# Kernel optimization log

Hardware: AMD Instinct MI355X
Metric: run time of the kernel (lower is better)

The kernel has to match this reference:

```python
import jax, jax.numpy as jnp
import numpy as np


def setup_inputs() -> dict:
    key = jax.random.key(0)
    ks = jax.random.split(key, 7)
    B, T, F, H = 512, 512, 64, 128
    s = 1.0 / np.sqrt(H)
    return {
        "x": jax.random.normal(ks[0], (B, T, F), dtype=jnp.float32),
        "W_ih": jax.random.uniform(ks[1], (3 * H, F), jnp.float32, -s, s),
        "W_hh": jax.random.uniform(ks[2], (3 * H, H), jnp.float32, -s, s),
        "b_ih": jax.random.uniform(ks[3], (3 * H,), jnp.float32, -s, s),
        "b_hh": jax.random.uniform(ks[4], (3 * H,), jnp.float32, -s, s),
        "W_out": jax.random.uniform(ks[5], (1, H), jnp.float32, -s, s),
        "b_out": jax.random.uniform(ks[6], (1,), jnp.float32, -s, s),
    }


def reference(x, W_ih, W_hh, b_ih, b_hh, W_out, b_out):
    B, T, F = x.shape
    H = W_hh.shape[1]
    # Precompute input projections for all timesteps: [T, B, 3H]
    x_t = jnp.transpose(x, (1, 0, 2))
    gi_all = jnp.einsum('tbf,gf->tbg', x_t, W_ih) + b_ih
    h0 = jnp.zeros((B, H), dtype=x.dtype)

    def step(h, gi):
        gh = h @ W_hh.T + b_hh  # [B, 3H]
        i_r, i_z, i_n = jnp.split(gi, 3, axis=-1)
        h_r, h_z, h_n = jnp.split(gh, 3, axis=-1)
        r = jax.nn.sigmoid(i_r + h_r)
        z = jax.nn.sigmoid(i_z + h_z)
        n = jnp.tanh(i_n + r * h_n)
        h_new = (1.0 - z) * n + z * h
        out = jnp.tanh(h_new @ W_out.T + b_out)[:, 0]  # [B]
        return h_new, out

    _, outs = jax.lax.scan(step, h0, gi_all)  # outs: [T, B]
    return outs.T  # [B, T]
```

## Files before the change

kernel.cpp:

```cpp
#include <hip/hip_runtime.h>
#include <math.h>

#define TSEQ 512
#define FDIM 64
#define HDIM 128
#define NB   512

#define SR 1.4426950408889634f
#define SN 2.8853900817779268f

typedef _Float16 f16x8 __attribute__((ext_vector_type(8)));
typedef _Float16 f16x4 __attribute__((ext_vector_type(4)));
typedef __fp16  fp16x2 __attribute__((ext_vector_type(2)));
typedef __attribute__((ext_vector_type(4))) float f32x4;

#define H_ROW 136
#define H_BUF (16 * H_ROW)

#if __has_builtin(__builtin_amdgcn_mfma_f32_16x16x16f16)
#define HAVE_MFMA16K16 1
__device__ __forceinline__ f32x4 mfma16k16(f16x4 a, f16x4 b, f32x4 c) {
    return __builtin_amdgcn_mfma_f32_16x16x16f16(a, b, c, 0, 0, 0);
}
#elif __has_builtin(__builtin_amdgcn_mfma_f32_16x16x16_f16)
#define HAVE_MFMA16K16 1
__device__ __forceinline__ f32x4 mfma16k16(f16x4 a, f16x4 b, f32x4 c) {
    return __builtin_amdgcn_mfma_f32_16x16x16_f16(a, b, c, 0, 0, 0);
}
#else
#define HAVE_MFMA16K16 0
#endif

__device__ __forceinline__ float exp2_hw(float x) {
#if __has_builtin(__builtin_amdgcn_exp2f)
    return __builtin_amdgcn_exp2f(x);
#else
    return exp2f(x);
#endif
}
__device__ __forceinline__ float fast_tanh(float x) {
    return 1.0f - 2.0f * __builtin_amdgcn_rcpf(1.0f + exp2_hw(SN * x));
}
__device__ __forceinline__ f32x4 mfma16f(f16x8 a, f16x8 b, f32x4 c) {
    return __builtin_amdgcn_mfma_f32_16x16x32_f16(a, b, c, 0, 0, 0);
}

union PU { fp16x2 h2[4]; f16x8 v; };
union GU { uint2 u; _Float16 h[4]; f16x4 v; };

__device__ __forceinline__ f16x8 pack_f16(float4 a, float4 b) {
    PU u;
    u.h2[0] = __builtin_amdgcn_cvt_pkrtz(a.x, a.y);
    u.h2[1] = __builtin_amdgcn_cvt_pkrtz(a.z, a.w);
    u.h2[2] = __builtin_amdgcn_cvt_pkrtz(b.x, b.y);
    u.h2[3] = __builtin_amdgcn_cvt_pkrtz(b.z, b.w);
    return u.v;
}

__device__ __forceinline__ void wg_barrier() {
    __builtin_amdgcn_sched_barrier(0);
    asm volatile("s_waitcnt lgkmcnt(0)" ::: "memory");
    __builtin_amdgcn_s_barrier();
    asm volatile("" ::: "memory");
    __builtin_amdgcn_sched_barrier(0);
}

__device__ __forceinline__ void gates(float a0v, float a1v, float a2v, float a3v,
                                      float& h_old, float wout, float& psum,
                                      _Float16& h16) {
    float r = __builtin_amdgcn_rcpf(1.0f + exp2_hw(-a0v));
    float z = __builtin_amdgcn_rcpf(1.0f + exp2_hw(-a1v));
    float y = fmaf(r, a3v, a2v);
    float n = fmaf(-2.0f, __builtin_amdgcn_rcpf(1.0f + exp2_hw(y)), 1.0f);
    float hn = fmaf(z, h_old - n, n);
    h_old = hn;
    h16 = (_Float16)hn;
    psum = fmaf(wout, hn, psum);
}

__global__ __launch_bounds__(512)
void gi_gemm16(const float* __restrict__ x,
               const float* __restrict__ W_ih,
               const float* __restrict__ b_ih,
               const float* __restrict__ b_hh,
               uint2* __restrict__ gi)
{
    const int tid  = threadIdx.x;
    const int w    = tid >> 6;
    const int lane = tid & 63;
    const int g4   = lane >> 4;
    const int bcol = lane & 15;
    const int b0   = blockIdx.x * 16;
    const int t0   = blockIdx.y * 16;

    __shared__ __align__(16) _Float16 xt[16 * 1032 + 8];

    {
        const int bl = tid >> 5, q = tid & 31;
        const float* xp = x + ((size_t)(b0 + bl) * TSEQ + t0) * FDIM;
        _Float16* dst = &xt[bl * 1032];
        #pragma unroll
        for (int j = 0; j < 8; ++j) {
            float4 v = *(const float4*)(xp + j * 128 + q * 4);
            union { fp16x2 p[2]; uint2 u; } pu;
            pu.p[0] = __builtin_amdgcn_cvt_pkrtz(v.x, v.y);
            pu.p[1] = __builtin_amdgcn_cvt_pkrtz(v.z, v.w);
            *(uint2*)&dst[j * 128 + q * 4] = pu.u;
        }
    }

    f16x8 WihF[3][2];
    #pragma unroll
    for (int kd = 0; kd < 3; ++kd) {
        const float sc = (kd < 2) ? SR : SN;
        const int g = kd * 128 + w * 16 + bcol;
        #pragma unroll
        for (int kt = 0; kt < 2; ++kt) {
            const float* pw = W_ih + g * FDIM + kt * 32 + g4 * 8;
            f16x8 v;
            #pragma unroll
            for (int e = 0; e < 8; ++e) v[e] = (_Float16)(pw[e] * sc);
            WihF[kd][kt] = v;
        }
    }
    f32x4 biasR, biasZ, biasN;
    #pragma unroll
    for (int i = 0; i < 4; ++i) {
        const int gr = w * 16 + g4 * 4 + i;
        biasR[i] = (b_ih[gr]       + b_hh[gr])       * SR;
        biasZ[i] = (b_ih[128 + gr] + b_hh[128 + gr]) * SR;
        biasN[i] = b_ih[256 + gr] * SN;
    }
    __syncthreads();

    for (int tt = 0; tt < 16; ++tt) {
        const _Float16* xr = &xt[bcol * 1032 + tt * 64];
        f16x8 xf0 = *(const f16x8*)(xr + g4 * 8);
        f16x8 xf1 = *(const f16x8*)(xr + 32 + g4 * 8);

        f32x4 c0 = biasR, c1 = biasZ, c2 = biasN;
        c0 = mfma16f(WihF[0][0], xf0, c0);
        c0 = mfma16f(WihF[0][1], xf1, c0);
        c1 = mfma16f(WihF[1][0], xf0, c1);
        c1 = mfma16f(WihF[1][1], xf1, c1);
        c2 = mfma16f(WihF[2][0], xf0, c2);
        c2 = mfma16f(WihF[2][1], xf1, c2);

        GU g0, g1, g2;
        #pragma unroll
        for (int i = 0; i < 4; ++i) {
            g0.h[i] = (_Float16)c0[i];
            g1.h[i] = (_Float16)c1[i];
            g2.h[i] = (_Float16)c2[i];
        }
        const int t = t0 + tt;
        const size_t base = ((size_t)t * 96 + w * 4 + g4) * NB + (b0 + bcol);
        gi[base]           = g0.u;
        gi[base + 32 * NB] = g1.u;
        gi[base + 64 * NB] = g2.u;
    }
}

__global__ __launch_bounds__(512)
void out_final(const float* __restrict__ pp,
               const float* __restrict__ b_out,
               float* __restrict__ out)
{
    const int t = blockIdx.x;
    const int b = threadIdx.x;
    float acc = b_out[0];
    const float* p = pp + (size_t)t * 32 * NB + b;
    #pragma unroll
    for (int c = 0; c < 32; ++c) acc += p[(size_t)c * NB];
    out[(size_t)b * TSEQ + t] = fast_tanh(acc);
}

template<bool USE_GI>
__global__ __launch_bounds__(512, 2)
void gru_f16(const float* __restrict__ x,
             const float* __restrict__ W_ih,
             const float* __restrict__ W_hh,
             const float* __restrict__ b_ih,
             const float* __restrict__ b_hh,
             const float* __restrict__ W_out,
             const float* __restrict__ b_out,
             const uint2* __restrict__ gi,
             float* __restrict__ pp,
             float* __restrict__ out)
{
    const int tid  = threadIdx.x;
    const int wid  = tid >> 6;
    const int lane = tid & 63;
    const int g4   = lane >> 4;
    const int bcol = lane & 15;
    const int b0   = blockIdx.x * 16;

    __shared__ __align__(16) _Float16 h_s[3][16][H_ROW];
    __shared__ __align__(16) float ps_s[3][16][12];

    f16x8 WhhF[3][4];
    f16x8 WihF[3][2];
    #pragma unroll
    for (int kd = 0; kd < 3; ++kd) {
        const float sc = (kd < 2) ? SR : SN;
        const int g = kd * 128 + wid * 16 + bcol;
        #pragma unroll
        for (int kt = 0; kt < 4; ++kt) {
            const float* pw = W_hh + g * HDIM + kt * 32 + g4 * 8;
            f16x8 v;
            #pragma unroll
            for (int e = 0; e < 8; ++e) v[e] = (_Float16)(pw[e] * sc);
            WhhF[kd][kt] = v;
        }
        if constexpr (!USE_GI) {
            #pragma unroll
            for (int kt = 0; kt < 2; ++kt) {
                const float* pw = W_ih + g * FDIM + kt * 32 + g4 * 8;
                f16x8 v;
                #pragma unroll
                for (int e = 0; e < 8; ++e) v[e] = (_Float16)(pw[e] * sc);
                WihF[kd][kt] = v;
            }
        }
    }

    f16x4 iden;
    #pragma unroll
    for (int e = 0; e < 4; ++e)
        iden[e] = (bcol == g4 * 4 + e) ? (_Float16)1.0f : (_Float16)0.0f;
    const f32x4 zero4 = {0.f, 0.f, 0.f, 0.f};

    f32x4 biasR, biasZ, biasNI, biasNH;
    float wout_r[4], h_old[4];
    #pragma unroll
    for (int i = 0; i < 4; ++i) {
        const int gr = wid * 16 + g4 * 4 + i;
        if constexpr (!USE_GI) {
            biasR[i]  = (b_ih[gr]       + b_hh[gr])       * SR;
            biasZ[i]  = (b_ih[128 + gr] + b_hh[128 + gr]) * SR;
            biasNI[i] = b_ih[256 + gr] * SN;
        }
        biasNH[i] = b_hh[256 + gr] * SN;
        wout_r[i] = W_out[gr];
        h_old[i]  = 0.0f;
    }
    const float bout = b_out[0];

    {
        unsigned* hp = (unsigned*)&h_s[0][0][0];
        for (int i = tid; i < H_BUF / 2; i += 512) hp[i] = 0u;
    }

    const float* xb = x + (size_t)(b0 + bcol) * TSEQ * FDIM;
    float4 sA0, sA1, sA2, sA3, sB0, sB1, sB2, sB3;
    f16x8 xf0, xf1;
    GU r0s, z0s, n0s, r1s, z1s, n1s, r2s, z2s, n2s, r3s, z3s, n3s;
    const uint2* gB = nullptr;
    float* ppp = nullptr;

    if constexpr (USE_GI) {
        gB  = gi + ((size_t)wid * 4 + g4) * NB + (b0 + bcol);
        ppp = pp + ((size_t)wid * 4 + g4) * NB + (b0 + bcol);
        r0s.u = gB[0];                              z0s.u = gB[32 * NB];
        n0s.u = gB[64 * NB];
        r1s.u = gB[(size_t)96 * NB];                z1s.u = gB[(size_t)96 * NB + 32 * NB];
        n1s.u = gB[(size_t)96 * NB + 64 * NB];
        r2s.u = gB[(size_t)192 * NB];               z2s.u = gB[(size_t)192 * NB + 32 * NB];
        n2s.u = gB[(size_t)192 * NB + 64 * NB];
        r3s.u = gB[(size_t)288 * NB];               z3s.u = gB[(size_t)288 * NB + 32 * NB];
        n3s.u = gB[(size_t)288 * NB + 64 * NB];
    } else {
        sA0 = *(const float4*)(xb + g4 * 8);
        sA1 = *(const float4*)(xb + g4 * 8 + 4);
        sA2 = *(const float4*)(xb + 32 + g4 * 8);
        sA3 = *(const float4*)(xb + 32 + g4 * 8 + 4);
        const float* xp1 = xb + FDIM;
        sB0 = *(const float4*)(xp1 + g4 * 8);
        sB1 = *(const float4*)(xp1 + g4 * 8 + 4);
        sB2 = *(const float4*)(xp1 + 32 + g4 * 8);
        sB3 = *(const float4*)(xp1 + 32 + g4 * 8 + 4);
        xf0 = pack_f16(sA0, sA1);
        xf1 = pack_f16(sA2, sA3);
    }

    __syncthreads();

    const bool outw = (!USE_GI) && (wid == 0) && (lane < 16);
    float* outp = out + (size_t)(b0 + lane) * TSEQ;
    float o0 = 0.f, o1 = 0.f, o2 = 0.f, o3 = 0.f;
    int rb = 0, wb = 1;

#if HAVE_MFMA16K16
#define GI_INJECT(RS, ZS, NS)                                               \
    a0 = mfma16k16(iden, RS.v, zero4);                                      \
    a1 = mfma16k16(iden, ZS.v, zero4);                                      \
    a2 = mfma16k16(iden, NS.v, zero4);
#else
#define GI_INJECT(RS, ZS, NS)                                               \
    a0 = (f32x4){(float)RS.h[0], (float)RS.h[1],                            \
                 (float)RS.h[2], (float)RS.h[3]};                           \
    a1 = (f32x4){(float)ZS.h[0], (float)ZS.h[1],                            \
                 (float)ZS.h[2], (float)ZS.h[3]};                           \
    a2 = (f32x4){(float)NS.h[0], (float)NS.h[1],                            \
                 (float)NS.h[2], (float)NS.h[3]};
#endif

#define GI_STEP(RS, ZS, NS)                                                 \
    GI_INJECT(RS, ZS, NS)                                                   \
    if (s + 4 < TSEQ) {                                                     \
        const size_t gof = (size_t)(s + 4) * 96 * NB;                       \
        RS.u = gB[gof];                                                     \
        ZS.u = gB[gof + 32 * NB];                                           \
        NS.u = gB[gof + 64 * NB];                                           \
    }

    for (int t = 0; t < TSEQ; t += 4) {
        #pragma unroll
        for (int u = 0; u < 4; ++u) {
            const int s = t + u;

            if (outw && s > 0) {
                f32x4 q0 = *(const f32x4*)&ps_s[rb][lane][0];
                f32x4 q1 = *(const f32x4*)&ps_s[rb][lane][4];
                float sm = (q0[0] + q0[1]) + (q0[2] + q0[3])
                         + (q1[0] + q1[1]) + (q1[2] + q1[3]);
                float val = fast_tanh(sm + bout);
                if (u == 0) {
                    o3 = val;
                    *(float4*)(outp + (t - 4)) = make_float4(o0, o1, o2, o3);
                } else if (u == 1) o0 = val;
                else if (u == 2) o1 = val;
                else o2 = val;
            }

            f32x4 a0, a1, a2, a3;

            f16x8 bh0 = *(const f16x8*)&h_s[rb][bcol][0 * 32 + g4 * 8];
            f16x8 bh1 = *(const f16x8*)&h_s[rb][bcol][1 * 32 + g4 * 8];
            f16x8 bh2 = *(const f16x8*)&h_s[rb][bcol][2 * 32 + g4 * 8];
            f16x8 bh3 = *(const f16x8*)&h_s[rb][bcol][3 * 32 + g4 * 8];

            if constexpr (USE_GI) {
                if (u == 0)      { GI_STEP(r0s, z0s, n0s) }
                else if (u == 1) { GI_STEP(r1s, z1s, n1s) }
                else if (u == 2) { GI_STEP(r2s, z2s, n2s) }
                else             { GI_STEP(r3s, z3s, n3s) }
                a3 = biasNH;

                a0 = mfma16f(WhhF[0][0], bh0, a0);
                a1 = mfma16f(WhhF[1][0], bh0, a1);
                a3 = mfma16f(WhhF[2][0], bh0, a3);
                a0 = mfma16f(WhhF[0][1], bh1, a0);
                a1 = mfma16f(WhhF[1][1], bh1, a1);
                a3 = mfma16f(WhhF[2][1], bh1, a3);
                a0 = mfma16f(WhhF[0][2], bh2, a0);
                a1 = mfma16f(WhhF[1][2], bh2, a1);
                a3 = mfma16f(WhhF[2][2], bh2, a3);
                a0 = mfma16f(WhhF[0][3], bh3, a0);
                a1 = mfma16f(WhhF[1][3], bh3, a1);
                a3 = mfma16f(WhhF[2][3], bh3, a3);
            } else {
                {
                    const int tl = (s + 2 < TSEQ) ? (s + 2) : (TSEQ - 1);
                    const float* xp = xb + (size_t)tl * FDIM;
                    if ((u & 1) == 0) {
                        sA0 = *(const float4*)(xp + g4 * 8);
                        sA1 = *(const float4*)(xp + g4 * 8 + 4);
                        sA2 = *(const float4*)(xp + 32 + g4 * 8);
                        sA3 = *(const float4*)(xp + 32 + g4 * 8 + 4);
                    } else {
                        sB0 = *(const float4*)(xp + g4 * 8);
                        sB1 = *(const float4*)(xp + g4 * 8 + 4);
                        sB2 = *(const float4*)(xp + 32 + g4 * 8);
                        sB3 = *(const float4*)(xp + 32 + g4 * 8 + 4);
                    }
                }
                a0 = biasR; a1 = biasZ; a2 = biasNI; a3 = biasNH;
                a0 = mfma16f(WihF[0][0], xf0, a0);
                a0 = mfma16f(WihF[0][1], xf1, a0);
                a1 = mfma16f(WihF[1][0], xf0, a1);
                a1 = mfma16f(WihF[1][1], xf1, a1);
                a2 = mfma16f(WihF[2][0], xf0, a2);
                a2 = mfma16f(WihF[2][1], xf1, a2);

                a0 = mfma16f(WhhF[0][0], bh0, a0);
                a1 = mfma16f(WhhF[1][0], bh0, a1);
                a3 = mfma16f(WhhF[2][0], bh0, a3);
                a0 = mfma16f(WhhF[0][1], bh1, a0);
                a1 = mfma16f(WhhF[1][1], bh1, a1);
                a3 = mfma16f(WhhF[2][1], bh1, a3);
                a0 = mfma16f(WhhF[0][2], bh2, a0);
                a1 = mfma16f(WhhF[1][2], bh2, a1);
                a3 = mfma16f(WhhF[2][2], bh2, a3);
                a0 = mfma16f(WhhF[0][3], bh3, a0);
                a1 = mfma16f(WhhF[1][3], bh3, a1);
                a3 = mfma16f(WhhF[2][3], bh3, a3);
            }

            float psum = 0.0f;
            _Float16 h16[4];
            #pragma unroll
            for (int i = 0; i < 4; ++i)
                gates(a0[i], a1[i], a2[i], a3[i], h_old[i], wout_r[i],
                      psum, h16[i]);

            union { _Float16 h[4]; uint2 u; } hu;
            hu.h[0] = h16[0]; hu.h[1] = h16[1];
            hu.h[2] = h16[2]; hu.h[3] = h16[3];
            *(uint2*)&h_s[wb][bcol][wid * 16 + g4 * 4] = hu.u;

            if constexpr (USE_GI) {
                *ppp = psum;
                ppp += 32 * NB;
            } else {
                psum += __shfl_xor(psum, 16);
                psum += __shfl_xor(psum, 32);
                if (lane < 16) ps_s[wb][lane][wid] = psum;
            }

            if constexpr (!USE_GI) {
                if ((u & 1) == 0) {
                    xf0 = pack_f16(sB0, sB1);
                    xf1 = pack_f16(sB2, sB3);
                } else {
                    xf0 = pack_f16(sA0, sA1);
                    xf1 = pack_f16(sA2, sA3);
                }
            }

            wg_barrier();
            rb = wb; wb = (wb == 2) ? 0 : wb + 1;
        }
    }
#undef GI_STEP
#undef GI_INJECT

    if (outw) {
        f32x4 q0 = *(const f32x4*)&ps_s[2][lane][0];
        f32x4 q1 = *(const f32x4*)&ps_s[2][lane][4];
        float sm = (q0[0] + q0[1]) + (q0[2] + q0[3])
                 + (q1[0] + q1[1]) + (q1[2] + q1[3]);
        o3 = fast_tanh(sm + bout);
        *(float4*)(outp + (TSEQ - 4)) = make_float4(o0, o1, o2, o3);
    }
}

extern "C" void kernel_launch(void* const* d_in, const int* in_sizes, int n_in,
                              void* d_out, int out_size, void* d_ws, size_t ws_size,
                              hipStream_t stream) {
    const float* x     = (const float*)d_in[0];
    const float* W_ih  = (const float*)d_in[1];
    const float* W_hh  = (const float*)d_in[2];
    const float* b_ih  = (const float*)d_in[3];
    const float* b_hh  = (const float*)d_in[4];
    const float* W_out = (const float*)d_in[5];
    const float* b_out = (const float*)d_in[6];
    float* out = (float*)d_out;

    const size_t gi_bytes = (size_t)TSEQ * NB * 384 * sizeof(_Float16);
    const size_t pp_bytes = (size_t)TSEQ * 32 * NB * sizeof(float);

    if (ws_size >= gi_bytes + pp_bytes) {
        uint2* gi = (uint2*)d_ws;
        float* pp = (float*)((char*)d_ws + gi_bytes);
        gi_gemm16<<<dim3(32, 32), 512, 0, stream>>>(x, W_ih, b_ih, b_hh, gi);
        gru_f16<true><<<32, 512, 0, stream>>>(x, W_ih, W_hh, b_ih, b_hh,
                                              W_out, b_out, gi, pp, out);
        out_final<<<TSEQ, NB, 0, stream>>>(pp, b_out, out);
    } else {
        gru_f16<false><<<32, 512, 0, stream>>>(x, W_ih, W_hh, b_ih, b_hh,
                                               W_out, b_out, nullptr, nullptr, out);
    }
}
```

Before: 345.0 us.

## Split GRU recurrence across 16 waves: r/z gate waves and n/update waves

The recurrent kernel now runs 1024 threads per block. Eight waves compute the r and z gate matmuls and sigmoids and pass them through shared memory. The other eight waves compute the n-gate matmul and the hidden-state update. This aims to shorten the serial per-step critical path by spreading the MFMA and transcendental work over twice as many waves. In exchange each step needs two workgroup barriers instead of one plus a shared-memory round trip, which may cost more than the parallelism saves. The fallback path is kept as a separate non-templated kernel.

```diff
diff --git a/kernel.cpp b/kernel.cpp
--- a/kernel.cpp
+++ b/kernel.cpp
@@ -16,6 +16,7 @@
 
 #define H_ROW 136
 #define H_BUF (16 * H_ROW)
+#define S_ROW 260
 
 #if __has_builtin(__builtin_amdgcn_mfma_f32_16x16x16f16)
 #define HAVE_MFMA16K16 1
@@ -63,19 +64,6 @@
     __builtin_amdgcn_s_barrier();
     asm volatile("" ::: "memory");
     __builtin_amdgcn_sched_barrier(0);
-}
-
-__device__ __forceinline__ void gates(float a0v, float a1v, float a2v, float a3v,
-                                      float& h_old, float wout, float& psum,
-                                      _Float16& h16) {
-    float r = __builtin_amdgcn_rcpf(1.0f + exp2_hw(-a0v));
-    float z = __builtin_amdgcn_rcpf(1.0f + exp2_hw(-a1v));
-    float y = fmaf(r, a3v, a2v);
-    float n = fmaf(-2.0f, __builtin_amdgcn_rcpf(1.0f + exp2_hw(y)), 1.0f);
-    float hn = fmaf(z, h_old - n, n);
-    h_old = hn;
-    h16 = (_Float16)hn;
-    psum = fmaf(wout, hn, psum);
 }
 
 __global__ __launch_bounds__(512)
@@ -175,18 +163,12 @@
     out[(size_t)b * TSEQ + t] = fast_tanh(acc);
 }
 
-template<bool USE_GI>
-__global__ __launch_bounds__(512, 2)
-void gru_f16(const float* __restrict__ x,
-             const float* __restrict__ W_ih,
-             const float* __restrict__ W_hh,
-             const float* __restrict__ b_ih,
-             const float* __restrict__ b_hh,
-             const float* __restrict__ W_out,
-             const float* __restrict__ b_out,
-             const uint2* __restrict__ gi,
-             float* __restrict__ pp,
-             float* __restrict__ out)
+__global__ __launch_bounds__(1024, 4)
+void gru_split(const float* __restrict__ W_hh,
+               const float* __restrict__ b_hh,
+               const float* __restrict__ W_out,
+               const uint2* __restrict__ gi,
+               float* __restrict__ pp)
 {
     const int tid  = threadIdx.x;
     const int wid  = tid >> 6;
@@ -194,6 +176,193 @@
     const int g4   = lane >> 4;
     const int bcol = lane & 15;
     const int b0   = blockIdx.x * 16;
+    const bool is_main = (wid < 8);
+    const int w = wid & 7;
+
+    __shared__ __align__(16) _Float16 h_s[3][16][H_ROW];
+    __shared__ __align__(16) float sig_s[3][16][S_ROW];
+
+    f16x4 iden;
+    #pragma unroll
+    for (int e = 0; e < 4; ++e)
+        iden[e] = (bcol == g4 * 4 + e) ? (_Float16)1.0f : (_Float16)0.0f;
+    const f32x4 zero4 = {0.f, 0.f, 0.f, 0.f};
+
+    f16x8 WhhA[4], WhhB[4];
+    f32x4 biasNH = zero4;
+    float wout_r[4], h_old[4];
+    if (is_main) {
+        const int g = 256 + w * 16 + bcol;
+        #pragma unroll
+        for (int kt = 0; kt < 4; ++kt) {
+            const float* pw = W_hh + g * HDIM + kt * 32 + g4 * 8;
+            f16x8 v;
+            #pragma unroll
+            for (int e = 0; e < 8; ++e) v[e] = (_Float16)(pw[e] * SN);
+            WhhA[kt] = v;
+        }
+        #pragma unroll
+        for (int i = 0; i < 4; ++i) {
+            const int gr = w * 16 + g4 * 4 + i;
+            biasNH[i] = b_hh[256 + gr] * SN;
+            wout_r[i] = W_out[gr];
+            h_old[i]  = 0.0f;
+        }
+    } else {
+        const int gr_ = w * 16 + bcol;
+        const int gz_ = 128 + w * 16 + bcol;
+        #pragma unroll
+        for (int kt = 0; kt < 4; ++kt) {
+            const float* pr = W_hh + gr_ * HDIM + kt * 32 + g4 * 8;
+            const float* pz = W_hh + gz_ * HDIM + kt * 32 + g4 * 8;
+            f16x8 vr, vz;
+            #pragma unroll
+            for (int e = 0; e < 8; ++e) {
+                vr[e] = (_Float16)(pr[e] * SR);
+                vz[e] = (_Float16)(pz[e] * SR);
+            }
+            WhhA[kt] = vr; WhhB[kt] = vz;
+        }
+    }
+
+    {
+        unsigned* hp = (unsigned*)&h_s[0][0][0];
+        for (int i = tid; i < H_BUF / 2; i += 1024) hp[i] = 0u;
+    }
+
+    GU a0s, a1s, a2s, a3s;
+    GU b0s, b1s, b2s, b3s;
+    const uint2* gA;
+    const uint2* gZ = nullptr;
+    float* ppp = nullptr;
+    if (is_main) {
+        gA  = gi + (size_t)(64 + w * 4 + g4) * NB + (b0 + bcol);
+        ppp = pp + (size_t)(w * 4 + g4) * NB + (b0 + bcol);
+    } else {
+        gA = gi + (size_t)(w * 4 + g4) * NB + (b0 + bcol);
+        gZ = gA + (size_t)32 * NB;
+    }
+    a0s.u = gA[0];
+    a1s.u = gA[(size_t)96  * NB];
+    a2s.u = gA[(size_t)192 * NB];
+    a3s.u = gA[(size_t)288 * NB];
+    if (!is_main) {
+        b0s.u = gZ[0];
+        b1s.u = gZ[(size_t)96  * NB];
+        b2s.u = gZ[(size_t)192 * NB];
+        b3s.u = gZ[(size_t)288 * NB];
+    }
+
+    __syncthreads();
+
+    const int sigoff = (w * 4 + g4) * 8;
+    int rb = 0, wb = 1;
+
+#if HAVE_MFMA16K16
+#define INJ(S) mfma16k16(iden, S.v, zero4)
+#else
+#define INJ(S) (f32x4){(float)S.h[0], (float)S.h[1], (float)S.h[2], (float)S.h[3]}
+#endif
+#define RFA(S) if (s + 4 < TSEQ) S.u = gA[(size_t)(s + 4) * 96 * NB];
+#define RFZ(S) if (s + 4 < TSEQ) S.u = gZ[(size_t)(s + 4) * 96 * NB];
+
+    for (int t = 0; t < TSEQ; t += 4) {
+        #pragma unroll
+        for (int u = 0; u < 4; ++u) {
+            const int s = t + u;
+
+            f16x8 bh0 = *(const f16x8*)&h_s[rb][bcol][0 * 32 + g4 * 8];
+            f16x8 bh1 = *(const f16x8*)&h_s[rb][bcol][1 * 32 + g4 * 8];
+            f16x8 bh2 = *(const f16x8*)&h_s[rb][bcol][2 * 32 + g4 * 8];
+            f16x8 bh3 = *(const f16x8*)&h_s[rb][bcol][3 * 32 + g4 * 8];
+
+            f32x4 a2 = zero4, a3 = zero4;
+
+            if (is_main) {
+                if (u == 0)      { a2 = INJ(a0s); RFA(a0s) }
+                else if (u == 1) { a2 = INJ(a1s); RFA(a1s) }
+                else if (u == 2) { a2 = INJ(a2s); RFA(a2s) }
+                else             { a2 = INJ(a3s); RFA(a3s) }
+                a3 = biasNH;
+                a3 = mfma16f(WhhA[0], bh0, a3);
+                a3 = mfma16f(WhhA[1], bh1, a3);
+                a3 = mfma16f(WhhA[2], bh2, a3);
+                a3 = mfma16f(WhhA[3], bh3, a3);
+            } else {
+                f32x4 a0, a1;
+                if (u == 0)      { a0 = INJ(a0s); a1 = INJ(b0s); RFA(a0s) RFZ(b0s) }
+                else if (u == 1) { a0 = INJ(a1s); a1 = INJ(b1s); RFA(a1s) RFZ(b1s) }
+                else if (u == 2) { a0 = INJ(a2s); a1 = INJ(b2s); RFA(a2s) RFZ(b2s) }
+                else             { a0 = INJ(a3s); a1 = INJ(b3s); RFA(a3s) RFZ(b3s) }
+                a0 = mfma16f(WhhA[0], bh0, a0);
+                a1 = mfma16f(WhhB[0], bh0, a1);
+                a0 = mfma16f(WhhA[1], bh1, a0);
+                a1 = mfma16f(WhhB[1], bh1, a1);
+                a0 = mfma16f(WhhA[2], bh2, a0);
+                a1 = mfma16f(WhhB[2], bh2, a1);
+                a0 = mfma16f(WhhA[3], bh3, a0);
+                a1 = mfma16f(WhhB[3], bh3, a1);
+                f32x4 rv, zv;
+                #pragma unroll
+                for (int i = 0; i < 4; ++i) {
+                    rv[i] = __builtin_amdgcn_rcpf(1.0f + exp2_hw(-a0[i]));
+                    zv[i] = __builtin_amdgcn_rcpf(1.0f + exp2_hw(-a1[i]));
+                }
+                *(f32x4*)&sig_s[wb][bcol][sigoff]     = rv;
+                *(f32x4*)&sig_s[wb][bcol][sigoff + 4] = zv;
+            }
+
+            wg_barrier();
+
+            if (is_main) {
+                f32x4 rv = *(const f32x4*)&sig_s[wb][bcol][sigoff];
+                f32x4 zv = *(const f32x4*)&sig_s[wb][bcol][sigoff + 4];
+                float psum = 0.0f;
+                _Float16 h16[4];
+                #pragma unroll
+                for (int i = 0; i < 4; ++i) {
+                    float y  = fmaf(rv[i], a3[i], a2[i]);
+                    float n  = fmaf(-2.0f,
+                                    __builtin_amdgcn_rcpf(1.0f + exp2_hw(y)),
+                                    1.0f);
+                    float hn = fmaf(zv[i], h_old[i] - n, n);
+                    h_old[i] = hn;
+                    h16[i]   = (_Float16)hn;
+                    psum = fmaf(wout_r[i], hn, psum);
+                }
+                union { _Float16 h[4]; uint2 u; } hu;
+                hu.h[0] = h16[0]; hu.h[1] = h16[1];
+                hu.h[2] = h16[2]; hu.h[3] = h16[3];
+                *(uint2*)&h_s[wb][bcol][w * 16 + g4 * 4] = hu.u;
+                *ppp = psum;
+                ppp += 32 * NB;
+            }
+
+            wg_barrier();
+            rb = wb; wb = (wb == 2) ? 0 : wb + 1;
+        }
+    }
+#undef INJ
+#undef RFA
+#undef RFZ
+}
+
+__global__ __launch_bounds__(512, 2)
+void gru_fb(const float* __restrict__ x,
+            const float* __restrict__ W_ih,
+            const float* __restrict__ W_hh,
+            const float* __restrict__ b_ih,
+            const float* __restrict__ b_hh,
+            const float* __restrict__ W_out,
+            const float* __restrict__ b_out,
+            float* __restrict__ out)
+{
+    const int tid  = threadIdx.x;
+    const int wid  = tid >> 6;
+    const int lane = tid & 63;
+    const int g4   = lane >> 4;
+    const int bcol = lane & 15;
+    const int b0   = blockIdx.x * 16;
 
     __shared__ __align__(16) _Float16 h_s[3][16][H_ROW];
     __shared__ __align__(16) float ps_s[3][16][12];
@@ -212,34 +381,24 @@
             for (int e = 0; e < 8; ++e) v[e] = (_Float16)(pw[e] * sc);
             WhhF[kd][kt] = v;
         }
-        if constexpr (!USE_GI) {
+        #pragma unroll
+        for (int kt = 0; kt < 2; ++kt) {
+            const float* pw = W_ih + g * FDIM + kt * 32 + g4 * 8;
+            f16x8 v;
             #pragma unroll
-            for (int kt = 0; kt < 2; ++kt) {
-                const float* pw = W_ih + g * FDIM + kt * 32 + g4 * 8;
-                f16x8 v;
-                #pragma unroll
-                for (int e = 0; e < 8; ++e) v[e] = (_Float16)(pw[e] * sc);
-                WihF[kd][kt] = v;
-            }
-        }
-    }
-
-    f16x4 iden;
-    #pragma unroll
-    for (int e = 0; e < 4; ++e)
-        iden[e] = (bcol == g4 * 4 + e) ? (_Float16)1.0f : (_Float16)0.0f;
-    const f32x4 zero4 = {0.f, 0.f, 0.f, 0.f};
+            for (int e = 0; e < 8; ++e) v[e] = (_Float16)(pw[e] * sc);
+            WihF[kd][kt] = v;
+        }
+    }
 
     f32x4 biasR, biasZ, biasNI, biasNH;
     float wout_r[4], h_old[4];
     #pragma unroll
     for (int i = 0; i < 4; ++i) {
         const int gr = wid * 16 + g4 * 4 + i;
-        if constexpr (!USE_GI) {
-            biasR[i]  = (b_ih[gr]       + b_hh[gr])       * SR;
-            biasZ[i]  = (b_ih[128 + gr] + b_hh[128 + gr]) * SR;
-            biasNI[i] = b_ih[256 + gr] * SN;
-        }
+        biasR[i]  = (b_ih[gr]       + b_hh[gr])       * SR;
+        biasZ[i]  = (b_ih[128 + gr] + b_hh[128 + gr]) * SR;
+        biasNI[i] = b_ih[256 + gr] * SN;
         biasNH[i] = b_hh[256 + gr] * SN;
         wout_r[i] = W_out[gr];
         h_old[i]  = 0.0f;
@@ -253,66 +412,26 @@
 
     const float* xb = x + (size_t)(b0 + bcol) * TSEQ * FDIM;
     float4 sA0, sA1, sA2, sA3, sB0, sB1, sB2, sB3;
-    f16x8 xf0, xf1;
-    GU r0s, z0s, n0s, r1s, z1s, n1s, r2s, z2s, n2s, r3s, z3s, n3s;
-    const uint2* gB = nullptr;
-    float* ppp = nullptr;
-
-    if constexpr (USE_GI) {
-        gB  = gi + ((size_t)wid * 4 + g4) * NB + (b0 + bcol);
-        ppp = pp + ((size_t)wid * 4 + g4) * NB + (b0 + bcol);
-        r0s.u = gB[0];                              z0s.u = gB[32 * NB];
-        n0s.u = gB[64 * NB];
-        r1s.u = gB[(size_t)96 * NB];                z1s.u = gB[(size_t)96 * NB + 32 * NB];
-        n1s.u = gB[(size_t)96 * NB + 64 * NB];
-        r2s.u = gB[(size_t)192 * NB];               z2s.u = gB[(size_t)192 * NB + 32 * NB];
-        n2s.u = gB[(size_t)192 * NB + 64 * NB];
-        r3s.u = gB[(size_t)288 * NB];               z3s.u = gB[(size_t)288 * NB + 32 * NB];
-        n3s.u = gB[(size_t)288 * NB + 64 * NB];
-    } else {
-        sA0 = *(const float4*)(xb + g4 * 8);
-        sA1 = *(const float4*)(xb + g4 * 8 + 4);
-        sA2 = *(const float4*)(xb + 32 + g4 * 8);
-        sA3 = *(const float4*)(xb + 32 + g4 * 8 + 4);
+    sA0 = *(const float4*)(xb + g4 * 8);
+    sA1 = *(const float4*)(xb + g4 * 8 + 4);
+    sA2 = *(const float4*)(xb + 32 + g4 * 8);
+    sA3 = *(const float4*)(xb + 32 + g4 * 8 + 4);
+    {
         const float* xp1 = xb + FDIM;
         sB0 = *(const float4*)(xp1 + g4 * 8);
         sB1 = *(const float4*)(xp1 + g4 * 8 + 4);
         sB2 = *(const float4*)(xp1 + 32 + g4 * 8);
         sB3 = *(const float4*)(xp1 + 32 + g4 * 8 + 4);
-        xf0 = pack_f16(sA0, sA1);
-        xf1 = pack_f16(sA2, sA3);
-    }
+    }
+    f16x8 xf0 = pack_f16(sA0, sA1);
+    f16x8 xf1 = pack_f16(sA2, sA3);
 
     __syncthreads();
 
-    const bool outw = (!USE_GI) && (wid == 0) && (lane < 16);
+    const bool outw = (wid == 0) && (lane < 16);
     float* outp = out + (size_t)(b0 + lane) * TSEQ;
     float o0 = 0.f, o1 = 0.f, o2 = 0.f, o3 = 0.f;
     int rb = 0, wb = 1;
-
-#if HAVE_MFMA16K16
-#define GI_INJECT(RS, ZS, NS)                                               \
-    a0 = mfma16k16(iden, RS.v, zero4);                                      \
-    a1 = mfma16k16(iden, ZS.v, zero4);                                      \
-    a2 = mfma16k16(iden, NS.v, zero4);
-#else
-#define GI_INJECT(RS, ZS, NS)                                               \
-    a0 = (f32x4){(float)RS.h[0], (float)RS.h[1],                            \
-                 (float)RS.h[2], (float)RS.h[3]};                           \
-    a1 = (f32x4){(float)ZS.h[0], (float)ZS.h[1],                            \
-                 (float)ZS.h[2], (float)ZS.h[3]};                           \
-    a2 = (f32x4){(float)NS.h[0], (float)NS.h[1],                            \
-                 (float)NS.h[2], (float)NS.h[3]};
-#endif
-
-#define GI_STEP(RS, ZS, NS)                                                 \
-    GI_INJECT(RS, ZS, NS)                                                   \
-    if (s + 4 < TSEQ) {                                                     \
-        const size_t gof = (size_t)(s + 4) * 96 * NB;                       \
-        RS.u = gB[gof];                                                     \
-        ZS.u = gB[gof + 32 * NB];                                           \
-        NS.u = gB[gof + 64 * NB];                                           \
-    }
 
     for (int t = 0; t < TSEQ; t += 4) {
         #pragma unroll
@@ -333,107 +452,83 @@
                 else o2 = val;
             }
 
-            f32x4 a0, a1, a2, a3;
-
+            {
+                const int tl = (s + 2 < TSEQ) ? (s + 2) : (TSEQ - 1);
+                const float* xp = xb + (size_t)tl * FDIM;
+                if ((u & 1) == 0) {
+                    sA0 = *(const float4*)(xp + g4 * 8);
+                    sA1 = *(const float4*)(xp + g4 * 8 + 4);
+                    sA2 = *(const float4*)(xp + 32 + g4 * 8);
+                    sA3 = *(const float4*)(xp + 32 + g4 * 8 + 4);
+                } else {
+                    sB0 = *(const float4*)(xp + g4 * 8);
+                    sB1 = *(const float4*)(xp + g4 * 8 + 4);
+                    sB2 = *(const float4*)(xp + 32 + g4 * 8);
+                    sB3 = *(const float4*)(xp + 32 + g4 * 8 + 4);
+                }
+            }
             f16x8 bh0 = *(const f16x8*)&h_s[rb][bcol][0 * 32 + g4 * 8];
             f16x8 bh1 = *(const f16x8*)&h_s[rb][bcol][1 * 32 + g4 * 8];
             f16x8 bh2 = *(const f16x8*)&h_s[rb][bcol][2 * 32 + g4 * 8];
             f16x8 bh3 = *(const f16x8*)&h_s[rb][bcol][3 * 32 + g4 * 8];
 
-            if constexpr (USE_GI) {
-                if (u == 0)      { GI_STEP(r0s, z0s, n0s) }
-                else if (u == 1) { GI_STEP(r1s, z1s, n1s) }
-                else if (u == 2) { GI_STEP(r2s, z2s, n2s) }
-                else             { GI_STEP(r3s, z3s, n3s) }
-                a3 = biasNH;
-
-                a0 = mfma16f(WhhF[0][0], bh0, a0);
-                a1 = mfma16f(WhhF[1][0], bh0, a1);
-                a3 = mfma16f(WhhF[2][0], bh0, a3);
-                a0 = mfma16f(WhhF[0][1], bh1, a0);
-                a1 = mfma16f(WhhF[1][1], bh1, a1);
-                a3 = mfma16f(WhhF[2][1], bh1, a3);
-                a0 = mfma16f(WhhF[0][2], bh2, a0);
-                a1 = mfma16f(WhhF[1][2], bh2, a1);
-                a3 = mfma16f(WhhF[2][2], bh2, a3);
-                a0 = mfma16f(WhhF[0][3], bh3, a0);
-                a1 = mfma16f(WhhF[1][3], bh3, a1);
-                a3 = mfma16f(WhhF[2][3], bh3, a3);
-            } else {
-                {
-                    const int tl = (s + 2 < TSEQ) ? (s + 2) : (TSEQ - 1);
-                    const float* xp = xb + (size_t)tl * FDIM;
-                    if ((u & 1) == 0) {
-                        sA0 = *(const float4*)(xp + g4 * 8);
-                        sA1 = *(const float4*)(xp + g4 * 8 + 4);
-                        sA2 = *(const float4*)(xp + 32 + g4 * 8);
-                        sA3 = *(const float4*)(xp + 32 + g4 * 8 + 4);
-                    } else {
-                        sB0 = *(const float4*)(xp + g4 * 8);
-                        sB1 = *(const float4*)(xp + g4 * 8 + 4);
-                        sB2 = *(const float4*)(xp + 32 + g4 * 8);
-                        sB3 = *(const float4*)(xp + 32 + g4 * 8 + 4);
-                    }
-                }
-                a0 = biasR; a1 = biasZ; a2 = biasNI; a3 = biasNH;
-                a0 = mfma16f(WihF[0][0], xf0, a0);
-                a0 = mfma16f(WihF[0][1], xf1, a0);
-                a1 = mfma16f(WihF[1][0], xf0, a1);
-                a1 = mfma16f(WihF[1][1], xf1, a1);
-                a2 = mfma16f(WihF[2][0], xf0, a2);
-                a2 = mfma16f(WihF[2][1], xf1, a2);
-
-                a0 = mfma16f(WhhF[0][0], bh0, a0);
-                a1 = mfma16f(WhhF[1][0], bh0, a1);
-                a3 = mfma16f(WhhF[2][0], bh0, a3);
-                a0 = mfma16f(WhhF[0][1], bh1, a0);
-                a1 = mfma16f(WhhF[1][1], bh1, a1);
-                a3 = mfma16f(WhhF[2][1], bh1, a3);
-                a0 = mfma16f(WhhF[0][2], bh2, a0);
-                a1 = mfma16f(WhhF[1][2], bh2, a1);
-                a3 = mfma16f(WhhF[2][2], bh2, a3);
-                a0 = mfma16f(WhhF[0][3], bh3, a0);
-                a1 = mfma16f(WhhF[1][3], bh3, a1);
-                a3 = mfma16f(WhhF[2][3], bh3, a3);
-            }
+            f32x4 a0 = biasR, a1 = biasZ, a2 = biasNI, a3 = biasNH;
+            a0 = mfma16f(WihF[0][0], xf0, a0);
+            a0 = mfma16f(WihF[0][1], xf1, a0);
+            a1 = mfma16f(WihF[1][0], xf0, a1);
+            a1 = mfma16f(WihF[1][1], xf1, a1);
+            a2 = mfma16f(WihF[2][0], xf0, a2);
+            a2 = mfma16f(WihF[2][1], xf1, a2);
+
+            a0 = mfma16f(WhhF[0][0], bh0, a0);
+            a1 = mfma16f(WhhF[1][0], bh0, a1);
+            a3 = mfma16f(WhhF[2][0], bh0, a3);
+            a0 = mfma16f(WhhF[0][1], bh1, a0);
+            a1 = mfma16f(WhhF[1][1], bh1, a1);
+            a3 = mfma16f(WhhF[2][1], bh1, a3);
+            a0 = mfma16f(WhhF[0][2], bh2, a0);
+            a1 = mfma16f(WhhF[1][2], bh2, a1);
+            a3 = mfma16f(WhhF[2][2], bh2, a3);
+            a0 = mfma16f(WhhF[0][3], bh3, a0);
+            a1 = mfma16f(WhhF[1][3], bh3, a1);
+            a3 = mfma16f(WhhF[2][3], bh3, a3);
 
             float psum = 0.0f;
             _Float16 h16[4];
             #pragma unroll
-            for (int i = 0; i < 4; ++i)
-                gates(a0[i], a1[i], a2[i], a3[i], h_old[i], wout_r[i],
-                      psum, h16[i]);
+            for (int i = 0; i < 4; ++i) {
+                float r  = __builtin_amdgcn_rcpf(1.0f + exp2_hw(-a0[i]));
+                float z  = __builtin_amdgcn_rcpf(1.0f + exp2_hw(-a1[i]));
+                float y  = fmaf(r, a3[i], a2[i]);
+                float n  = fmaf(-2.0f,
+                                __builtin_amdgcn_rcpf(1.0f + exp2_hw(y)), 1.0f);
+                float hn = fmaf(z, h_old[i] - n, n);
+                h_old[i] = hn;
+                h16[i]   = (_Float16)hn;
+                psum = fmaf(wout_r[i], hn, psum);
+            }
 
             union { _Float16 h[4]; uint2 u; } hu;
             hu.h[0] = h16[0]; hu.h[1] = h16[1];
             hu.h[2] = h16[2]; hu.h[3] = h16[3];
             *(uint2*)&h_s[wb][bcol][wid * 16 + g4 * 4] = hu.u;
 
-            if constexpr (USE_GI) {
-                *ppp = psum;
-                ppp += 32 * NB;
+            psum += __shfl_xor(psum, 16);
+            psum += __shfl_xor(psum, 32);
+            if (lane < 16) ps_s[wb][lane][wid] = psum;
+
+            if ((u & 1) == 0) {
+                xf0 = pack_f16(sB0, sB1);
+                xf1 = pack_f16(sB2, sB3);
             } else {
-                psum += __shfl_xor(psum, 16);
-                psum += __shfl_xor(psum, 32);
-                if (lane < 16) ps_s[wb][lane][wid] = psum;
-            }
-
-            if constexpr (!USE_GI) {
-                if ((u & 1) == 0) {
-                    xf0 = pack_f16(sB0, sB1);
-                    xf1 = pack_f16(sB2, sB3);
-                } else {
-                    xf0 = pack_f16(sA0, sA1);
-                    xf1 = pack_f16(sA2, sA3);
-                }
+                xf0 = pack_f16(sA0, sA1);
+                xf1 = pack_f16(sA2, sA3);
             }
 
             wg_barrier();
             rb = wb; wb = (wb == 2) ? 0 : wb + 1;
         }
     }
-#undef GI_STEP
-#undef GI_INJECT
 
     if (outw) {
         f32x4 q0 = *(const f32x4*)&ps_s[2][lane][0];
@@ -464,11 +559,10 @@
         uint2* gi = (uint2*)d_ws;
         float* pp = (float*)((char*)d_ws + gi_bytes);
         gi_gemm16<<<dim3(32, 32), 512, 0, stream>>>(x, W_ih, b_ih, b_hh, gi);
-        gru_f16<true><<<32, 512, 0, stream>>>(x, W_ih, W_hh, b_ih, b_hh,
-                                              W_out, b_out, gi, pp, out);
+        gru_split<<<32, 1024, 0, stream>>>(W_hh, b_hh, W_out, gi, pp);
         out_final<<<TSEQ, NB, 0, stream>>>(pp, b_out, out);
     } else {
-        gru_f16<false><<<32, 512, 0, stream>>>(x, W_ih, W_hh, b_ih, b_hh,
-                                               W_out, b_out, nullptr, nullptr, out);
-    }
-}
+        gru_fb<<<32, 512, 0, stream>>>(x, W_ih, W_hh, b_ih, b_hh,
+                                       W_out, b_out, out);
+    }
+}
```

Result: slower. 481.9 us (+39.7%).
